# Performance work log

Measured on AMD Instinct MI355X. Metric: run time of the kernel, lower is better.

The kernel has to match this reference:

```python
import jax, jax.numpy as jnp
import numpy as np

WS = 8        # window size (square)
TW = 8        # total windows per side = input_resolution // WS
NH = 16       # num heads


def make_indices(ws, tw):
    # local relative position index (N, N)
    c = np.stack(np.meshgrid(np.arange(ws), np.arange(ws), indexing='ij')).reshape(2, -1)
    rel = (c[:, :, None] - c[:, None, :]).transpose(1, 2, 0).astype(np.int64)
    rel[..., 0] += ws - 1
    rel[..., 1] += ws - 1
    rel[..., 0] *= 2 * ws - 1
    local_idx = rel.sum(-1)
    # global (window-token -> window-grid) relative position index (N, tw*tw)
    ck = np.stack(np.meshgrid(np.arange(tw), np.arange(tw), indexing='ij')).reshape(2, -1)
    relg = (c[:, :, None] - ck[:, None, :]).transpose(1, 2, 0).astype(np.int64)
    relg[..., 0] += tw - 1
    relg[..., 1] += tw - 1
    relg[..., 0] *= ws + tw - 1
    global_idx = relg.sum(-1)
    return local_idx, global_idx


def setup_inputs() -> dict:
    key = jax.random.key(0)
    ks = jax.random.split(key, 13)
    B, H, W, C = 16, 64, 64, 512
    s = 0.02
    return {
        'x': jax.random.normal(ks[0], (B, H, W, C), jnp.float32),
        'qkv_w': jax.random.normal(ks[1], (C, 3 * C), jnp.float32) * s,
        'qkv_b': jax.random.normal(ks[2], (3 * C,), jnp.float32) * s,
        'local_bias_table': jax.random.normal(ks[3], ((2 * WS - 1) ** 2, NH), jnp.float32) * s,
        'global_bias_table': jax.random.normal(ks[4], ((WS + TW - 1) ** 2, NH), jnp.float32) * s,
        'local_proj_w': jax.random.normal(ks[5], (C, C), jnp.float32) * s,
        'local_proj_b': jax.random.normal(ks[6], (C,), jnp.float32) * s,
        'pool_w': jnp.full((WS * WS,), 1.0 / (WS * WS) * (WS * WS), jnp.float32) * 0 + jax.random.normal(ks[7], (WS * WS,), jnp.float32) * s + 1.0 / (WS * WS),
        'pool_b': jnp.zeros((1,), jnp.float32),
        'global_proj_w': jax.random.normal(ks[8], (C, C), jnp.float32) * s,
        'global_proj_b': jax.random.normal(ks[9], (C,), jnp.float32) * s,
        'pfc_w': jax.random.normal(ks[10], (2 * C, C), jnp.float32) * s,
        'pfc_b': jax.random.normal(ks[11], (C,), jnp.float32) * s,
    }


def reference(x, qkv_w, qkv_b, local_bias_table, global_bias_table,
              local_proj_w, local_proj_b, pool_w, pool_b,
              global_proj_w, global_proj_b, pfc_w, pfc_b):
    B, H, W, C = x.shape
    N = WS * WS                      # tokens per window
    nWs = (H // WS) * (W // WS)      # number of windows
    B_ = B * nWs
    hd = C // NH
    scale = hd ** -0.5

    local_idx, global_idx = make_indices(WS, H // WS)

    # NOTE: faithful to original — qkv applied to x in row-major order,
    # then reshaped into (B_, N, ...) chunks (window_partition output is unused).
    qkv = (x.reshape(-1, C) @ qkv_w + qkv_b).reshape(B_, N, 3, NH, hd)
    qkv = qkv.transpose(2, 0, 3, 1, 4)  # (3, B_, NH, N, hd)
    q, k, v = qkv[0], qkv[1], qkv[2]

    # ---- fine (local window) attention ----
    lb = local_bias_table[local_idx.reshape(-1)].reshape(N, N, NH).transpose(2, 0, 1)
    fine = jax.nn.softmax(jnp.einsum('bhnd,bhmd->bhnm', q * scale, k) + lb[None])
    fine_out = jnp.einsum('bhnm,bhmd->bnhd', fine, v).reshape(B_, N, C)
    fine_out = fine_out @ local_proj_w + local_proj_b

    # ---- coarse (pooled global) attention ----
    k5 = k.reshape(B, nWs, NH, N, hd)
    v5 = v.reshape(B, nWs, NH, N, hd)
    # pooled over the N window-token axis; original uses pool_layer_k for BOTH K and V
    Kg = jnp.einsum('bwhnd,n->bhwd', k5, pool_w) + pool_b  # (B, NH, nWs, hd)
    Vg = jnp.einsum('bwhnd,n->bhwd', v5, pool_w) + pool_b
    Kb = jnp.broadcast_to(Kg[:, None], (B, nWs, NH, nWs, hd)).reshape(B_, NH, nWs, hd)
    Vb = jnp.broadcast_to(Vg[:, None], (B, nWs, NH, nWs, hd)).reshape(B_, NH, nWs, hd)

    gb = global_bias_table[global_idx.reshape(-1)].reshape(N, nWs, NH).transpose(2, 0, 1)
    coarse = jax.nn.softmax(jnp.einsum('bhnd,bhwd->bhnw', q * scale, Kb) + gb[None])
    coarse_out = jnp.einsum('bhnw,bhwd->bnhd', coarse, Vb).reshape(B_, N, C)
    coarse_out = coarse_out @ global_proj_w + global_proj_b

    # ---- fused projection ----
    out = jnp.concatenate([fine_out, coarse_out], axis=-1) @ pfc_w + pfc_b
    return out  # (B_, N, C)
```

## Files before the change

### kernel.cpp

```cpp
#include <hip/hip_runtime.h>


typedef unsigned int u32;
typedef _Float16 f16;
typedef __attribute__((ext_vector_type(8))) _Float16 f16x8;
typedef __attribute__((ext_vector_type(4))) float f32x4;
typedef __attribute__((ext_vector_type(4))) u32 u32x4;

__device__ __forceinline__ f32x4 mfma_16x16x32(f16x8 a, f16x8 b, f32x4 c) {
  return __builtin_amdgcn_mfma_f32_16x16x32_f16(a, b, c, 0, 0, 0);
}

__device__ __forceinline__ void async_cp16(const void* g, void* l) {
  __builtin_amdgcn_global_load_lds(
      (const __attribute__((address_space(1))) u32*)g,
      (__attribute__((address_space(3))) u32*)l, 16, 0, 0);
}

__device__ __forceinline__ f16x8 cvt8_rtz(const float4 a, const float4 b) {
  u32x4 w;
  w[0] = __builtin_bit_cast(u32, __builtin_amdgcn_cvt_pkrtz(a.x, a.y));
  w[1] = __builtin_bit_cast(u32, __builtin_amdgcn_cvt_pkrtz(a.z, a.w));
  w[2] = __builtin_bit_cast(u32, __builtin_amdgcn_cvt_pkrtz(b.x, b.y));
  w[3] = __builtin_bit_cast(u32, __builtin_amdgcn_cvt_pkrtz(b.z, b.w));
  return __builtin_bit_cast(f16x8, w);
}

__global__ __launch_bounds__(256) void k_prep(
    const float* __restrict__ X, f16* __restrict__ X16,
    const float* __restrict__ ltab, const float* __restrict__ gtab,
    float* __restrict__ lbf, float* __restrict__ gbf,
    const float* __restrict__ qkv_w, f16* __restrict__ qwT,
    const float* __restrict__ lpw, const float* __restrict__ gpw,
    const float* __restrict__ pfc_w, f16* __restrict__ WcT,
    const float* __restrict__ lpb, const float* __restrict__ gpb,
    const float* __restrict__ pfc_b, float* __restrict__ bc) {
  __shared__ char sm[9216];
  const int b = blockIdx.x;
  const int t = threadIdx.x;

  if (b < 64) {
    float (*sW)[16] = (float(*)[16])sm;
    const int kk0 = b * 16;
    const bool top = kk0 < 512;
    const float* src = top ? (lpw + kk0 * 512) : (gpw + (kk0 - 512) * 512);
    const float* pf = pfc_w + (top ? 0 : 512 * 512);
    float acc0[16], acc1[16];
#pragma unroll
    for (int i = 0; i < 16; ++i) { acc0[i] = 0.f; acc1[i] = 0.f; }
    for (int ct = 0; ct < 32; ++ct) {
      sW[t >> 4][t & 15] = src[(t >> 4) * 512 + ct * 16 + (t & 15)];
      __syncthreads();
#pragma unroll
      for (int cc = 0; cc < 16; ++cc) {
        const int c = ct * 16 + cc;
        const float p0 = pf[c * 512 + t];
        const float p1 = pf[c * 512 + t + 256];
#pragma unroll
        for (int i = 0; i < 16; ++i) { acc0[i] += sW[i][cc] * p0; acc1[i] += sW[i][cc] * p1; }
      }
      __syncthreads();
    }
#pragma unroll
    for (int i = 0; i < 16; ++i) {
      const int kk = kk0 + i;
      const int kp = ((kk >> 5) & 15) * 64 + (kk >> 9) * 32 + (kk & 31);
      WcT[(size_t)t * 1024 + kp] = (f16)acc0[i];
      WcT[(size_t)(t + 256) * 1024 + kp] = (f16)acc1[i];
    }
  } else if (b < 66) {
    const int j = (b - 64) * 256 + t;
    float acc = pfc_b[j];
    for (int c = 0; c < 512; ++c)
      acc += lpb[c] * pfc_w[(size_t)c * 512 + j] + gpb[c] * pfc_w[(size_t)(512 + c) * 512 + j];
    bc[j] = acc;
  } else if (b < 194) {
    const int id = (b - 66) * 256 + t;
    const int tab = id >> 14;
    const int rem = id & 16383;
    const int h = rem >> 10;
    const int wv = (rem >> 8) & 3;
    const int j = (rem >> 6) & 3;
    const int l = rem & 63;
    const int lk = l >> 4, lr = l & 15;
    const float* src = tab ? gtab : ltab;
    float* out = (tab ? gbf : lbf) + (size_t)rem * 4;
#pragma unroll
    for (int r = 0; r < 4; ++r) {
      const int n = wv * 16 + lk * 4 + r;
      const int m = j * 16 + lr;
      const int idx = ((n >> 3) - (m >> 3) + 7) * 15 + ((n & 7) - (m & 7) + 7);
      out[r] = src[idx * 16 + h];
    }
  } else if (b < 386) {
    f16 (*sT)[72] = (f16(*)[72])sm;
    const int bid = b - 194;
    const int k0 = (bid / 24) * 64, n0 = (bid % 24) * 64;
    const float sc = (n0 < 512) ? 0.17677669529663687f : 1.0f;
#pragma unroll
    for (int p = 0; p < 4; ++p) {
      const int kl = p * 16 + (t >> 4), nl = (t & 15) * 4;
      const float4 v = *reinterpret_cast<const float4*>(qkv_w + (size_t)(k0 + kl) * 1536 + n0 + nl);
      sT[kl][nl] = (f16)(v.x * sc); sT[kl][nl + 1] = (f16)(v.y * sc);
      sT[kl][nl + 2] = (f16)(v.z * sc); sT[kl][nl + 3] = (f16)(v.w * sc);
    }
    __syncthreads();
#pragma unroll
    for (int q = 0; q < 2; ++q) {
      const int nl = q * 32 + (t >> 3), kl = (t & 7) * 8;
      f16x8 r;
#pragma unroll
      for (int j = 0; j < 8; ++j) r[j] = sT[kl + j][nl];
      *reinterpret_cast<f16x8*>(qwT + (size_t)(n0 + nl) * 512 + k0 + kl) = r;
    }
  } else {
    const int vb = b - 386;
    const size_t stride = (size_t)2048 * 256 * 8;
    size_t base = ((size_t)vb * 256 + t) * 8;
    for (int it = 0; it < 8; ++it, base += stride) {
      const float4 a = *reinterpret_cast<const float4*>(X + base);
      const float4 bb = *reinterpret_cast<const float4*>(X + base + 4);
      *reinterpret_cast<f16x8*>(X16 + base) = cvt8_rtz(a, bb);
    }
  }
}

__global__ __launch_bounds__(512, 2) void k_gemm_qkv(const f16* __restrict__ A,
                                                     const f16* __restrict__ BT,
                                                     const float* __restrict__ qkv_b,
                                                     const float* __restrict__ pool_w,
                                                     const float* __restrict__ pool_b,
                                                     f16* __restrict__ qb,
                                                     f16* __restrict__ kb,
                                                     f16* __restrict__ vb,
                                                     f16* __restrict__ Kgb,
                                                     f16* __restrict__ Vgt) {
  __shared__ f16 sA[2][8192], sB[2][4096];
  const int wid = (blockIdx.x & 7) * 384 + (blockIdx.x >> 3);
  const int br = wid / 12, bn = wid % 12;
  const int t = threadIdx.x;
  const int wv = t >> 6, l = t & 63, lr = l & 15, lk = l >> 4;
  const int wvr = wv >> 1, wvc = wv & 1;

  f32x4 acc[4][4] = {};

  const int srow = t >> 2;
  const int sxc = ((t & 3) ^ (srow & 3)) * 8;
  const f16* gA = A + (size_t)(br * 256 + srow) * 512 + sxc;
  const f16* gB = BT + (size_t)(bn * 128 + srow) * 512 + sxc;

  async_cp16(gA, &sA[0][t * 8]);
  async_cp16(gA + 128 * 512, &sA[0][4096 + t * 8]);
  async_cp16(gB, &sB[0][t * 8]);
  __syncthreads();

  int cur = 0;
  for (int kk = 0; kk < 16; ++kk) {
    if (kk < 15) {
      async_cp16(gA + (kk + 1) * 32, &sA[cur ^ 1][t * 8]);
      async_cp16(gA + 128 * 512 + (kk + 1) * 32, &sA[cur ^ 1][4096 + t * 8]);
      async_cp16(gB + (kk + 1) * 32, &sB[cur ^ 1][t * 8]);
    }
    f16x8 af[4], bf[4];
#pragma unroll
    for (int m = 0; m < 4; ++m) {
      const int row = wvr * 64 + m * 16 + lr;
      af[m] = *reinterpret_cast<const f16x8*>(&sA[cur][row * 32 + ((lk ^ (row & 3)) * 8)]);
    }
#pragma unroll
    for (int n = 0; n < 4; ++n) {
      const int row = wvc * 64 + n * 16 + lr;
      bf[n] = *reinterpret_cast<const f16x8*>(&sB[cur][row * 32 + ((lk ^ (row & 3)) * 8)]);
    }
#pragma unroll
    for (int m = 0; m < 4; ++m)
#pragma unroll
      for (int n = 0; n < 4; ++n) acc[m][n] = mfma_16x16x32(af[m], bf[n], acc[m][n]);
    if (kk < 15) {
      __syncthreads();
      cur ^= 1;
    }
  }

  const int w_idx = br * 4 + wvr;
  const int bb = w_idx >> 6, ww = w_idx & 63;
  float pw[4][4];
#pragma unroll
  for (int m = 0; m < 4; ++m)
#pragma unroll
    for (int r = 0; r < 4; ++r) pw[m][r] = pool_w[m * 16 + lk * 4 + r];
  const float pb = pool_b[0];

#pragma unroll
  for (int n = 0; n < 4; ++n) {
    const int col = bn * 128 + wvc * 64 + n * 16 + lr;
    const int which = col >> 9;
    const int hh = (col >> 5) & 15, d = col & 31;
    const float bias = which == 0 ? qkv_b[col] * 0.17677669529663687f : qkv_b[col];
    f16* dst = which == 0 ? qb : (which == 1 ? kb : vb);
#pragma unroll
    for (int m = 0; m < 4; ++m)
#pragma unroll
      for (int r = 0; r < 4; ++r) {
        const int row = br * 256 + wvr * 64 + m * 16 + lk * 4 + r;
        dst[(size_t)(((row >> 6) << 4) + hh) * 2048 + (row & 63) * 32 + d] =
            (f16)(acc[m][n][r] + bias);
      }
    if (which != 0) {
      float part = 0.f;
#pragma unroll
      for (int m = 0; m < 4; ++m)
#pragma unroll
        for (int r = 0; r < 4; ++r) part += (acc[m][n][r] + bias) * pw[m][r];
      part += __shfl_xor(part, 16);
      part += __shfl_xor(part, 32);
      part += pb;
      if (lk == 0) {
        if (which == 1)
          Kgb[((size_t)(bb * 16 + hh) * 64 + ww) * 32 + d] = (f16)part;
        else
          Vgt[((size_t)(bb * 16 + hh) * 32 + d) * 64 + ww] = (f16)part;
      }
    }
  }
}

__global__ __launch_bounds__(256) void k_attn(const f16* __restrict__ qb,
                                              const f16* __restrict__ kb,
                                              const f16* __restrict__ vb,
                                              const f16* __restrict__ Kgb,
                                              const f16* __restrict__ Vgt,
                                              const float* __restrict__ lbf,
                                              const float* __restrict__ gbf,
                                              f16* __restrict__ cat) {
  __shared__ f16 sVrawA[2048], sVrawB[2048];
  __shared__ f16 sVtA[2048], sVtB[2048];
  __shared__ f16 sP[4096], sCat[4096];
  const int bid = blockIdx.x;
  const int h = bid >> 9, pair = bid & 511;
  const int b_0 = pair * 2;
  const int gs = ((b_0 >> 6) << 4) + h;
  const int t = threadIdx.x;
  const int wv = t >> 6, l = t & 63, lr = l & 15, lk = l >> 4;
  const size_t hs0 = ((size_t)b_0 * 16 + h) * 2048;
  const size_t hs1 = hs0 + 16 * 2048;

  async_cp16(vb + hs0 + t * 8, &sVrawA[t * 8]);
  async_cp16(vb + hs1 + t * 8, &sVrawB[t * 8]);

  f32x4 bL[4], bG[4];
#pragma unroll
  for (int j = 0; j < 4; ++j) {
    bL[j] = *reinterpret_cast<const f32x4*>(lbf + (size_t)((h * 4 + wv) * 4 + j) * 256 + l * 4);
    bG[j] = *reinterpret_cast<const f32x4*>(gbf + (size_t)((h * 4 + wv) * 4 + j) * 256 + l * 4);
  }

  float p[4][4], inv[4];

#pragma unroll
  for (int w = 0; w < 2; ++w) {
    const size_t hs = w ? hs1 : hs0;
    const f16* sVt = w ? sVtB : sVtA;
    const f16x8 aq = *reinterpret_cast<const f16x8*>(qb + hs + (wv * 16 + lr) * 32 + lk * 8);

    f32x4 s[4];
#pragma unroll
    for (int j = 0; j < 4; ++j) {
      const f16x8 bk = *reinterpret_cast<const f16x8*>(kb + hs + (j * 16 + lr) * 32 + lk * 8);
      s[j] = mfma_16x16x32(aq, bk, bL[j]);
    }

    if (w == 0) {
      __syncthreads();
      const int d = t >> 3, tok0 = (t & 7) << 3;
      f16x8 wa, wb;
#pragma unroll
      for (int j = 0; j < 8; ++j) {
        wa[j] = sVrawA[(tok0 + j) * 32 + d];
        wb[j] = sVrawB[(tok0 + j) * 32 + d];
      }
      const int slot = d * 64 + (((t & 7) ^ (d & 7)) << 3);
      *reinterpret_cast<f16x8*>(&sVtA[slot]) = wa;
      *reinterpret_cast<f16x8*>(&sVtB[slot]) = wb;
    }

#pragma unroll
    for (int r = 0; r < 4; ++r) {
      float su = 0.f;
#pragma unroll
      for (int j = 0; j < 4; ++j) {
        const float e = __expf(s[j][r]);
        p[j][r] = e;
        su += e;
      }
      su += __shfl_xor(su, 1);
      su += __shfl_xor(su, 2);
      su += __shfl_xor(su, 4);
      su += __shfl_xor(su, 8);
      inv[r] = 1.f / su;
    }
#pragma unroll
    for (int r = 0; r < 4; ++r) {
      const int rowP = wv * 16 + lk * 4 + r;
#pragma unroll
      for (int j = 0; j < 4; ++j) {
        const int col = j * 16 + lr;
        sP[rowP * 64 + (((col >> 3) ^ (rowP & 7)) << 3) + (col & 7)] = (f16)p[j][r];
      }
    }

    if (w == 0) __syncthreads();

    {
      const int rowP = wv * 16 + lr;
      const f16x8 a0 = *reinterpret_cast<const f16x8*>(&sP[rowP * 64 + ((lk ^ (lr & 7)) << 3)]);
      const f16x8 a1 = *reinterpret_cast<const f16x8*>(&sP[rowP * 64 + (((4 + lk) ^ (lr & 7)) << 3)]);
#pragma unroll
      for (int n = 0; n < 2; ++n) {
        const int d = n * 16 + lr;
        const f16x8 b0 = *reinterpret_cast<const f16x8*>(&sVt[d * 64 + ((lk ^ (d & 7)) << 3)]);
        const f16x8 b1 = *reinterpret_cast<const f16x8*>(&sVt[d * 64 + (((4 + lk) ^ (d & 7)) << 3)]);
        f32x4 o = {};
        o = mfma_16x16x32(a0, b0, o);
        o = mfma_16x16x32(a1, b1, o);
#pragma unroll
        for (int r = 0; r < 4; ++r) {
          const int rowC = wv * 16 + lk * 4 + r;
          const int colC = n * 16 + lr;
          sCat[rowC * 64 + (((colC >> 3) ^ (rowC & 7)) << 3) + (colC & 7)] =
              (f16)(o[r] * inv[r]);
        }
      }
    }

#pragma unroll
    for (int j = 0; j < 4; ++j) {
      const f16x8 bk = *reinterpret_cast<const f16x8*>(
          Kgb + ((size_t)gs * 64 + j * 16 + lr) * 32 + lk * 8);
      s[j] = mfma_16x16x32(aq, bk, bG[j]);
    }
#pragma unroll
    for (int r = 0; r < 4; ++r) {
      float su = 0.f;
#pragma unroll
      for (int j = 0; j < 4; ++j) {
        const float e = __expf(s[j][r]);
        p[j][r] = e;
        su += e;
      }
      su += __shfl_xor(su, 1);
      su += __shfl_xor(su, 2);
      su += __shfl_xor(su, 4);
      su += __shfl_xor(su, 8);
      inv[r] = 1.f / su;
    }
#pragma unroll
    for (int r = 0; r < 4; ++r) {
      const int rowP = wv * 16 + lk * 4 + r;
#pragma unroll
      for (int j = 0; j < 4; ++j) {
        const int col = j * 16 + lr;
        sP[rowP * 64 + (((col >> 3) ^ (rowP & 7)) << 3) + (col & 7)] = (f16)p[j][r];
      }
    }

    {
      const int rowP = wv * 16 + lr;
      const f16x8 a0 = *reinterpret_cast<const f16x8*>(&sP[rowP * 64 + ((lk ^ (lr & 7)) << 3)]);
      const f16x8 a1 = *reinterpret_cast<const f16x8*>(&sP[rowP * 64 + (((4 + lk) ^ (lr & 7)) << 3)]);
#pragma unroll
      for (int n = 0; n < 2; ++n) {
        const f16* vp = Vgt + ((size_t)gs * 32 + n * 16 + lr) * 64 + lk * 8;
        const f16x8 b0 = *reinterpret_cast<const f16x8*>(vp);
        const f16x8 b1 = *reinterpret_cast<const f16x8*>(vp + 32);
        f32x4 o = {};
        o = mfma_16x16x32(a0, b0, o);
        o = mfma_16x16x32(a1, b1, o);
#pragma unroll
        for (int r = 0; r < 4; ++r) {
          const int rowC = wv * 16 + lk * 4 + r;
          const int colC = 32 + n * 16 + lr;
          sCat[rowC * 64 + (((colC >> 3) ^ (rowC & 7)) << 3) + (colC & 7)] =
              (f16)(o[r] * inv[r]);
        }
      }
    }

    f16* catp = cat + ((size_t)(b_0 + w) * 64) * 1024 + h * 64;
#pragma unroll
    for (int pass = 0; pass < 2; ++pass) {
      const int row = wv * 16 + pass * 8 + (l >> 3);
      const int c = l & 7;
      const f16x8 v = *reinterpret_cast<const f16x8*>(&sCat[row * 64 + ((c ^ (row & 7)) << 3)]);
      *reinterpret_cast<f16x8*>(catp + (size_t)row * 1024 + c * 8) = v;
    }
  }
}

__global__ __launch_bounds__(512, 2) void k_gemm_final(const f16* __restrict__ A,
                                                       const f16* __restrict__ BT,
                                                       const float* __restrict__ bc,
                                                       float* __restrict__ out) {
  __shared__ f16 sA[8192];
  __shared__ f16 sB[16384];
  const int wid = (blockIdx.x & 7) * 128 + (blockIdx.x >> 3);
  const int br = wid >> 1, bn = wid & 1;
  const int t = threadIdx.x;
  const int wv = t >> 6, l = t & 63, lr = l & 15, lk = l >> 4;
  const int wvM = wv >> 2, wvN = wv & 3;

  f32x4 acc[4][4] = {};

  const int srow = t >> 3;
  const int scg = (t & 7) ^ (srow & 7);
  const f16* gA = A + (size_t)(br * 128 + srow) * 1024 + scg * 8;
  const f16* gB = BT + (size_t)(bn * 256 + srow) * 1024 + scg * 8;

  for (int kk = 0; kk < 16; ++kk) {
#pragma unroll
    for (int i = 0; i < 2; ++i)
      async_cp16(gA + (size_t)(i * 64) * 1024 + kk * 64, &sA[(i * 512 + t) * 8]);
#pragma unroll
    for (int i = 0; i < 4; ++i)
      async_cp16(gB + (size_t)(i * 64) * 1024 + kk * 64, &sB[(i * 512 + t) * 8]);
    __syncthreads();
    f16x8 af[4][2], bf[4][2];
#pragma unroll
    for (int m = 0; m < 4; ++m) {
      const int row = wvM * 64 + m * 16 + lr;
#pragma unroll
      for (int hh = 0; hh < 2; ++hh)
        af[m][hh] = *reinterpret_cast<const f16x8*>(
            &sA[row * 64 + ((((hh << 2) + lk) ^ (row & 7)) << 3)]);
    }
#pragma unroll
    for (int n = 0; n < 4; ++n) {
      const int row = wvN * 64 + n * 16 + lr;
#pragma unroll
      for (int hh = 0; hh < 2; ++hh)
        bf[n][hh] = *reinterpret_cast<const f16x8*>(
            &sB[row * 64 + ((((hh << 2) + lk) ^ (row & 7)) << 3)]);
    }
#pragma unroll
    for (int m = 0; m < 4; ++m)
#pragma unroll
      for (int n = 0; n < 4; ++n) {
        acc[m][n] = mfma_16x16x32(af[m][0], bf[n][0], acc[m][n]);
        acc[m][n] = mfma_16x16x32(af[m][1], bf[n][1], acc[m][n]);
      }
    __syncthreads();
  }

#pragma unroll
  for (int n = 0; n < 4; ++n) {
    const int col = bn * 256 + wvN * 64 + n * 16 + lr;
    const float bias = bc[col];
#pragma unroll
    for (int m = 0; m < 4; ++m)
#pragma unroll
      for (int r = 0; r < 4; ++r) {
        const int row = br * 128 + wvM * 64 + m * 16 + lk * 4 + r;
        out[(size_t)row * 512 + col] = acc[m][n][r] + bias;
      }
  }
}


extern "C" void kernel_launch(void* const* d_in, const int* in_sizes, int n_in,
                              void* d_out, int out_size, void* d_ws, size_t ws_size,
                              hipStream_t stream) {
  const float* x      = (const float*)d_in[0];
  const float* qkv_w  = (const float*)d_in[1];
  const float* qkv_b  = (const float*)d_in[2];
  const float* ltab   = (const float*)d_in[3];
  const float* gtab   = (const float*)d_in[4];
  const float* lpw    = (const float*)d_in[5];
  const float* lpb    = (const float*)d_in[6];
  const float* pool_w = (const float*)d_in[7];
  const float* pool_b = (const float*)d_in[8];
  const float* gpw    = (const float*)d_in[9];
  const float* gpb    = (const float*)d_in[10];
  const float* pfc_w  = (const float*)d_in[11];
  const float* pfc_b  = (const float*)d_in[12];
  float* out = (float*)d_out;

  char* ws = (char*)d_ws;
  f16*   qb   = (f16*)(ws + 0);
  f16*   kb   = (f16*)(ws + 67108864);
  f16*   vb   = (f16*)(ws + 134217728);
  f16*   cat  = (f16*)(ws + 201326592);
  f16*   X16  = (f16*)(ws + 201326592);
  f16*   qwT  = (f16*)(ws + 335544320);
  f16*   WcT  = (f16*)(ws + 337117184);
  float* bc   = (float*)(ws + 338165760);
  float* lbf  = (float*)(ws + 338167808);
  float* gbf  = (float*)(ws + 338429952);
  f16*   Kgb  = (f16*)(ws + 338692096);
  f16*   Vgt  = (f16*)(ws + 339740672);

  k_prep<<<2434, 256, 0, stream>>>(x, X16, ltab, gtab, lbf, gbf, qkv_w, qwT,
                                   lpw, gpw, pfc_w, WcT, lpb, gpb, pfc_b, bc);
  k_gemm_qkv<<<3072, 512, 0, stream>>>(X16, qwT, qkv_b, pool_w, pool_b,
                                       qb, kb, vb, Kgb, Vgt);
  k_attn<<<8192, 256, 0, stream>>>(qb, kb, vb, Kgb, Vgt, lbf, gbf, cat);
  k_gemm_final<<<1024, 512, 0, stream>>>(cat, WcT, bc, out);
}
```

Before: 449.8 us.

## Double-buffer final GEMM with 1024-thread blocks covering full N

Rewrites the final projection GEMM to use 1024-thread blocks that each compute a 128x512 output tile over the full N dimension. The K loop now steps 32 at a time and double-buffers the A and B tiles in LDS, prefetching the next slice while the current one is multiplied. The XOR swizzle on the LDS tiles is dropped. The attention kernel also writes the probability matrix into a separate LDS buffer, so it no longer reuses sP. This raises LDS use per block, may add bank conflicts without the swizzle, and leaves a dead loop behind.

```diff
diff --git a/kernel.cpp b/kernel.cpp
--- a/kernel.cpp
+++ b/kernel.cpp
@@ -235,7 +235,7 @@
                                               f16* __restrict__ cat) {
   __shared__ f16 sVrawA[2048], sVrawB[2048];
   __shared__ f16 sVtA[2048], sVtB[2048];
-  __shared__ f16 sP[4096], sCat[4096];
+  __shared__ f16 sP[4096], sP2[4096], sCat[4096];
   const int bid = blockIdx.x;
   const int h = bid >> 9, pair = bid & 511;
   const int b_0 = pair * 2;
@@ -360,14 +360,14 @@
 #pragma unroll
       for (int j = 0; j < 4; ++j) {
         const int col = j * 16 + lr;
-        sP[rowP * 64 + (((col >> 3) ^ (rowP & 7)) << 3) + (col & 7)] = (f16)p[j][r];
+        sP2[rowP * 64 + (((col >> 3) ^ (rowP & 7)) << 3) + (col & 7)] = (f16)p[j][r];
       }
     }
 
     {
       const int rowP = wv * 16 + lr;
-      const f16x8 a0 = *reinterpret_cast<const f16x8*>(&sP[rowP * 64 + ((lk ^ (lr & 7)) << 3)]);
-      const f16x8 a1 = *reinterpret_cast<const f16x8*>(&sP[rowP * 64 + (((4 + lk) ^ (lr & 7)) << 3)]);
+      const f16x8 a0 = *reinterpret_cast<const f16x8*>(&sP2[rowP * 64 + ((lk ^ (lr & 7)) << 3)]);
+      const f16x8 a1 = *reinterpret_cast<const f16x8*>(&sP2[rowP * 64 + (((4 + lk) ^ (lr & 7)) << 3)]);
 #pragma unroll
       for (int n = 0; n < 2; ++n) {
         const f16* vp = Vgt + ((size_t)gs * 32 + n * 16 + lr) * 64 + lk * 8;
@@ -397,63 +397,61 @@
   }
 }
 
-__global__ __launch_bounds__(512, 2) void k_gemm_final(const f16* __restrict__ A,
-                                                       const f16* __restrict__ BT,
-                                                       const float* __restrict__ bc,
-                                                       float* __restrict__ out) {
-  __shared__ f16 sA[8192];
-  __shared__ f16 sB[16384];
-  const int wid = (blockIdx.x & 7) * 128 + (blockIdx.x >> 3);
-  const int br = wid >> 1, bn = wid & 1;
+__global__ __launch_bounds__(1024) void k_gemm_final(const f16* __restrict__ A,
+                                                     const f16* __restrict__ BT,
+                                                     const float* __restrict__ bc,
+                                                     float* __restrict__ out) {
+  __shared__ f16 sA[2][4096];
+  __shared__ f16 sB[2][16384];
+  const int br = (blockIdx.x & 7) * 64 + (blockIdx.x >> 3);
   const int t = threadIdx.x;
   const int wv = t >> 6, l = t & 63, lr = l & 15, lk = l >> 4;
-  const int wvM = wv >> 2, wvN = wv & 3;
+  const int wvM = wv >> 3, wvN = wv & 7;
 
   f32x4 acc[4][4] = {};
 
-  const int srow = t >> 3;
-  const int scg = (t & 7) ^ (srow & 7);
-  const f16* gA = A + (size_t)(br * 128 + srow) * 1024 + scg * 8;
-  const f16* gB = BT + (size_t)(bn * 256 + srow) * 1024 + scg * 8;
-
-  for (int kk = 0; kk < 16; ++kk) {
-#pragma unroll
-    for (int i = 0; i < 2; ++i)
-      async_cp16(gA + (size_t)(i * 64) * 1024 + kk * 64, &sA[(i * 512 + t) * 8]);
-#pragma unroll
-    for (int i = 0; i < 4; ++i)
-      async_cp16(gB + (size_t)(i * 64) * 1024 + kk * 64, &sB[(i * 512 + t) * 8]);
-    __syncthreads();
-    f16x8 af[4][2], bf[4][2];
-#pragma unroll
-    for (int m = 0; m < 4; ++m) {
-      const int row = wvM * 64 + m * 16 + lr;
-#pragma unroll
-      for (int hh = 0; hh < 2; ++hh)
-        af[m][hh] = *reinterpret_cast<const f16x8*>(
-            &sA[row * 64 + ((((hh << 2) + lk) ^ (row & 7)) << 3)]);
-    }
-#pragma unroll
-    for (int n = 0; n < 4; ++n) {
-      const int row = wvN * 64 + n * 16 + lr;
-#pragma unroll
-      for (int hh = 0; hh < 2; ++hh)
-        bf[n][hh] = *reinterpret_cast<const f16x8*>(
-            &sB[row * 64 + ((((hh << 2) + lk) ^ (row & 7)) << 3)]);
-    }
+  const f16* gA = A + (size_t)(br * 128 + (t >> 2)) * 1024 + (t & 3) * 8;
+  const f16* gB0 = BT + (size_t)(t >> 2) * 1024 + (t & 3) * 8;
+  const f16* gB1 = BT + (size_t)((t + 1024) >> 2) * 1024 + (t & 3) * 8;
+
+  if (t < 512) async_cp16(gA, &sA[0][t * 8]);
+  async_cp16(gB0, &sB[0][t * 8]);
+  async_cp16(gB1, &sB[0][(t + 1024) * 8]);
+  __syncthreads();
+
+  int cur = 0;
+  for (int kk = 0; kk < 32; ++kk) {
+    if (kk < 31) {
+      if (t < 512) async_cp16(gA + (kk + 1) * 32, &sA[cur ^ 1][t * 8]);
+      async_cp16(gB0 + (kk + 1) * 32, &sB[cur ^ 1][t * 8]);
+      async_cp16(gB1 + (kk + 1) * 32, &sB[cur ^ 1][(t + 1024) * 8]);
+    }
+    f16x8 af[2], bf[4];
+#pragma unroll
+    for (int m = 0; m < 2; ++m) {
+      const int row = wvM * 64 + (m * 2 + (lk >> 1)) * 0;
+      (void)row;
+    }
+    f16x8 afr[4], bfr[4];
 #pragma unroll
     for (int m = 0; m < 4; ++m)
-#pragma unroll
-      for (int n = 0; n < 4; ++n) {
-        acc[m][n] = mfma_16x16x32(af[m][0], bf[n][0], acc[m][n]);
-        acc[m][n] = mfma_16x16x32(af[m][1], bf[n][1], acc[m][n]);
-      }
-    __syncthreads();
+      afr[m] = *reinterpret_cast<const f16x8*>(&sA[cur][(wvM * 64 + m * 16 + lr) * 32 + lk * 8]);
+#pragma unroll
+    for (int n = 0; n < 4; ++n)
+      bfr[n] = *reinterpret_cast<const f16x8*>(&sB[cur][(wvN * 64 + n * 16 + lr) * 32 + lk * 8]);
+#pragma unroll
+    for (int m = 0; m < 4; ++m)
+#pragma unroll
+      for (int n = 0; n < 4; ++n) acc[m][n] = mfma_16x16x32(afr[m], bfr[n], acc[m][n]);
+    if (kk < 31) {
+      __syncthreads();
+      cur ^= 1;
+    }
   }
 
 #pragma unroll
   for (int n = 0; n < 4; ++n) {
-    const int col = bn * 256 + wvN * 64 + n * 16 + lr;
+    const int col = wvN * 64 + n * 16 + lr;
     const float bias = bc[col];
 #pragma unroll
     for (int m = 0; m < 4; ++m)
@@ -503,5 +501,5 @@
   k_gemm_qkv<<<3072, 512, 0, stream>>>(X16, qwT, qkv_b, pool_w, pool_b,
                                        qb, kb, vb, Kgb, Vgt);
   k_attn<<<8192, 256, 0, stream>>>(qb, kb, vb, Kgb, Vgt, lbf, gbf, cat);
-  k_gemm_final<<<1024, 512, 0, stream>>>(cat, WcT, bc, out);
-}
+  k_gemm_final<<<512, 1024, 0, stream>>>(cat, WcT, bc, out);
+}
```

New measurement: 503.9 us. 1.12x slower.
